# Kernel tuning notes

Measured on AMD Instinct MI355X. Metric: run time of the kernel, lower is better.

The kernel has to match this reference:

```python
import jax, jax.numpy as jnp
import numpy as np

NQ = 4          # n_qubits
NL = 2          # n_layers
DIM = 2 ** NQ   # statevector dimension (16)
PI = np.float32(np.pi)

# H^{otimes NQ} (real, symmetric)
_H2 = np.array([[1.0, 1.0], [1.0, -1.0]], dtype=np.float32) / np.sqrt(2.0)
_M = _H2
for _ in range(NQ - 1):
    _M = np.kron(_M, _H2)
H_ALL = jnp.asarray(_M.astype(np.complex64))  # [DIM, DIM]

# z_i = +1/-1 eigenvalues per computational basis state; wire 0 is MSB (PennyLane)
_b = ((np.arange(DIM)[:, None] >> (NQ - 1 - np.arange(NQ))[None, :]) & 1)
Z = jnp.asarray((1.0 - 2.0 * _b).astype(np.float32))      # [DIM, NQ]
ZZ = Z[:, :-1] * Z[:, 1:]                                  # [DIM, NQ-1]


def _encode(angles):
    """Apply the ZZ feature map to |0...0>. angles: [..., NQ] -> state [..., DIM] complex64.

    Per layer: all Hadamards, then diagonal phase exp(-i/2 (sum th_i z_i + sum th_i th_{i+1} z_i z_{i+1}))
    (RZ and CNOT-RZ-CNOT = ZZ phase are diagonal; gates on distinct wires commute).
    """
    arg = (jnp.einsum('...q,dq->...d', angles, Z)
           + jnp.einsum('...p,dp->...d', angles[..., :-1] * angles[..., 1:], ZZ))
    diag = jnp.exp(arg * (-0.5j)).astype(jnp.complex64)     # [..., DIM]
    state = jnp.zeros(angles.shape[:-1] + (DIM,), jnp.complex64).at[..., 0].set(1.0)
    for _ in range(NL):
        state = state @ H_ALL      # H_ALL symmetric -> s @ H == H @ s
        state = state * diag
    return state


def setup_inputs() -> dict:
    key = jax.random.key(0)
    ks = jax.random.split(key, 7)
    B, L, S, H, D = 8, 1024, 1024, 8, 64
    return {
        'queries': jax.random.normal(ks[0], (B, L, H, D), jnp.float32),
        'keys':    jax.random.normal(ks[1], (B, S, H, D), jnp.float32),
        'values':  jax.random.normal(ks[2], (B, S, H, D), jnp.float32),
        'wq': jax.random.normal(ks[3], (NQ, D), jnp.float32) * 0.1,
        'bq': jax.random.normal(ks[4], (NQ,), jnp.float32) * 0.1,
        'wk': jax.random.normal(ks[5], (NQ, D), jnp.float32) * 0.1,
        'bk': jax.random.normal(ks[6], (NQ,), jnp.float32) * 0.1,
    }


def reference(queries, keys, values, wq, bq, wk, bk):
    # queries: [B,L,H,D], keys/values: [B,S,H,D]
    q_angles = jnp.tanh(queries @ wq.T + bq) * PI          # [B,L,H,NQ]
    k_angles = jnp.tanh(keys @ wk.T + bk) * PI             # [B,S,H,NQ]
    sq = _encode(q_angles.transpose(0, 2, 1, 3))           # [B,H,L,DIM] complex
    sk = _encode(k_angles.transpose(0, 2, 1, 3))           # [B,H,S,DIM] complex
    fid = jnp.einsum('bhld,bhsd->bhls', sq, jnp.conj(sk))  # overlap <phi_k|phi_q>
    attn_scores = (fid.real ** 2 + fid.imag ** 2).astype(queries.dtype)  # |.|^2 = probs[0]
    attn_weights = attn_scores / (attn_scores.sum(axis=-1, keepdims=True) + 1e-6)
    v = values.transpose(0, 2, 1, 3)                       # [B,H,S,D]
    context = jnp.einsum('bhls,bhsd->bhld', attn_weights, v).transpose(0, 2, 1, 3)
    return context, attn_weights
```

## Files before the change

### kernel.cpp

```cpp
#include <hip/hip_runtime.h>
#include <math.h>

#define PI_F 3.14159265358979323846f

constexpr int Bq = 8, Lq = 1024, Sq = 1024, Hq = 8, Dq = 64;

typedef short short8 __attribute__((ext_vector_type(8)));
typedef _Float16 half8 __attribute__((ext_vector_type(8)));
typedef float f4v __attribute__((ext_vector_type(4)));
typedef unsigned short ushort_t;

static __device__ __forceinline__ f4v mfma16h(half8 a, half8 b, f4v c) {
  return __builtin_amdgcn_mfma_f32_16x16x32_f16(a, b, c, 0, 0, 0);
}
static __device__ __forceinline__ half8 primefh(half8 q) {
  union { half8 h; short8 s; } in, out;
  in.h = q;
#pragma unroll
  for (int i = 0; i < 4; ++i) {
    out.s[2 * i]     = in.s[2 * i + 1];
    out.s[2 * i + 1] = (short)(((ushort_t)in.s[2 * i]) ^ 0x8000u);
  }
  return out.h;
}
static __device__ __forceinline__ unsigned pkh(float a, float b) {
  union { _Float16 h[2]; unsigned u; } p;
  p.h[0] = (_Float16)a; p.h[1] = (_Float16)b;
  return p.u;
}

static __device__ __forceinline__ void state_vec(
    const float* __restrict__ x, const float (*lw)[64], const float* lb,
    int n, float st[32])
{
  const float4* xp = (const float4*)(x + (size_t)n * 64);
  float a0 = lb[0], a1 = lb[1], a2 = lb[2], a3 = lb[3];
#pragma unroll
  for (int i = 0; i < 16; ++i) {
    float4 v = xp[i];
    a0 += v.x * lw[0][4*i] + v.y * lw[0][4*i+1] + v.z * lw[0][4*i+2] + v.w * lw[0][4*i+3];
    a1 += v.x * lw[1][4*i] + v.y * lw[1][4*i+1] + v.z * lw[1][4*i+2] + v.w * lw[1][4*i+3];
    a2 += v.x * lw[2][4*i] + v.y * lw[2][4*i+1] + v.z * lw[2][4*i+2] + v.w * lw[2][4*i+3];
    a3 += v.x * lw[3][4*i] + v.y * lw[3][4*i+1] + v.z * lw[3][4*i+2] + v.w * lw[3][4*i+3];
  }
  a0 = tanhf(a0) * PI_F; a1 = tanhf(a1) * PI_F;
  a2 = tanhf(a2) * PI_F; a3 = tanhf(a3) * PI_F;
  float p01 = a0 * a1, p12 = a1 * a2, p23 = a2 * a3;

  float dr[16], di[16];
#pragma unroll
  for (int d = 0; d < 16; ++d) {
    float s0 = (d & 8) ? -1.f : 1.f;
    float s1 = (d & 4) ? -1.f : 1.f;
    float s2 = (d & 2) ? -1.f : 1.f;
    float s3 = (d & 1) ? -1.f : 1.f;
    float arg = a0*s0 + a1*s1 + a2*s2 + a3*s3
              + p01*s0*s1 + p12*s1*s2 + p23*s2*s3;
    float sn, cs;
    sincosf(0.5f * arg, &sn, &cs);
    dr[d] = cs; di[d] = -sn;
  }
  float hr[16], hi[16];
#pragma unroll
  for (int i = 0; i < 16; ++i) { hr[i] = dr[i]; hi[i] = di[i]; }
#pragma unroll
  for (int stp = 1; stp < 16; stp <<= 1) {
#pragma unroll
    for (int i = 0; i < 16; ++i) {
      if (!(i & stp)) {
        float xr = hr[i], yr = hr[i + stp];
        hr[i] = xr + yr; hr[i + stp] = xr - yr;
        float xi = hi[i], yi = hi[i + stp];
        hi[i] = xi + yi; hi[i + stp] = xi - yi;
      }
    }
  }
#pragma unroll
  for (int d = 0; d < 16; ++d) {
    st[2*d]   = (dr[d] * hr[d] - di[d] * hi[d]) * 0.0625f;
    st[2*d+1] = (dr[d] * hi[d] + di[d] * hr[d]) * 0.0625f;
  }
}

__global__ __launch_bounds__(256) void k_prep(
    const float* __restrict__ qin, const float* __restrict__ kin,
    const float* __restrict__ vin,
    const float* __restrict__ wq, const float* __restrict__ bq,
    const float* __restrict__ wk, const float* __restrict__ bk,
    ushort_t* __restrict__ QF, ushort_t* __restrict__ KF,
    ushort_t* __restrict__ VF)
{
  __shared__ float smem[64 * 68];
  int blk = blockIdx.x;
  int t = threadIdx.x;

  if (blk < 512) {
    const bool isQ = (blk < 256);
    const float* x    = isQ ? qin : kin;
    const float* w    = isQ ? wq : wk;
    const float* bias = isQ ? bq : bk;
    float (*lw)[64] = (float(*)[64])smem;
    float* lb = smem + 256;
    lw[t >> 6][t & 63] = w[t];
    if (t < 4) lb[t] = bias[t];
    __syncthreads();

    int n = (blk & 255) * 256 + t;
    float st[32];
    state_vec(x, lw, lb, n, st);
    int b = n >> 13, l = (n >> 3) & 1023, h = n & 7;
    int bh = b * 8 + h;

    unsigned hp[16];
#pragma unroll
    for (int i = 0; i < 16; ++i) hp[i] = pkh(st[2*i], st[2*i+1]);

    if (isQ) {
      size_t rb = ((size_t)bh * Lq + l) * 32;
      uint4* ph = (uint4*)(QF + rb);
#pragma unroll
      for (int i = 0; i < 4; ++i)
        ph[i] = make_uint4(hp[4*i], hp[4*i+1], hp[4*i+2], hp[4*i+3]);
    } else {
      int sf = l >> 4, lh = l & 15;
      size_t fb = (size_t)(bh * 64 + sf) * 512;
#pragma unroll
      for (int g = 0; g < 4; ++g) {
        size_t o = fb + (size_t)((g << 4) + lh) * 8;
        *(uint4*)(KF + o) = make_uint4(hp[4*g], hp[4*g+1], hp[4*g+2], hp[4*g+3]);
      }
    }
  } else {
    int blk2 = blk - 512;
    int bh = blk2 >> 4, c = blk2 & 15;
    int b = bh >> 3, h = bh & 7;
    int s0 = c << 6;
    int sl = t >> 2, dq = (t & 3) << 4;
    const float4* src =
        (const float4*)(vin + (((size_t)b * Sq + s0 + sl) * Hq + h) * 64 + dq);
#pragma unroll
    for (int i = 0; i < 4; ++i)
      *(float4*)&smem[sl * 68 + dq + 4 * i] = src[i];
    __syncthreads();
#pragma unroll
    for (int sidx = 0; sidx < 2; ++sidx) {
      int slot = sidx * 256 + t;
      int ks = slot >> 8, f2 = (slot >> 6) & 3, lane = slot & 63;
      int lh = lane & 15, g = lane >> 4;
      int d = f2 * 16 + lh;
      unsigned w4[4];
#pragma unroll
      for (int e2 = 0; e2 < 4; ++e2) {
        int sl0 = ks * 32 + g * 8 + 2 * e2;
        w4[e2] = pkh(smem[sl0 * 68 + d], smem[(sl0 + 1) * 68 + d]);
      }
      size_t off = ((((size_t)(bh * 16 + c) * 2 + ks) * 4 + f2) * 64 + lane) * 8;
      *(uint4*)(VF + off) = make_uint4(w4[0], w4[1], w4[2], w4[3]);
    }
  }
}

__global__ __launch_bounds__(256, 4) void k_fidpv7(
    const ushort_t* __restrict__ QF, const ushort_t* __restrict__ KF,
    const ushort_t* __restrict__ VF, float* __restrict__ attn,
    float* __restrict__ ctx)
{
  __shared__ float Wtr[4][16 * 68];

  int bid = blockIdx.x;
  int xcd = bid & 7, idx = bid >> 3;
  int bh = (xcd << 3) | (idx >> 4);
  int l0 = (idx & 15) << 6;
  int t = threadIdx.x;
  int wv = t >> 6, lane = t & 63;
  int lh = lane & 15, g = lane >> 4, ko = g << 3;
  int rowbase = l0 + (wv << 4);

  size_t qoff = ((size_t)bh * Lq + rowbase + lh) * 32 + ko;
  half8 qf  = *(const half8*)(QF + qoff);
  half8 qpf = primefh(qf);

  const ushort_t* gK = KF + (size_t)bh * 32768 + (size_t)lane * 8;
  const ushort_t* gV = VF + (size_t)bh * 65536 + (size_t)lane * 8;

  f4v zero = {0.f, 0.f, 0.f, 0.f};

  float rsum = 0.f;
#pragma unroll 8
  for (int sf = 0; sf < 64; ++sf) {
    half8 kf = *(const half8*)(gK + sf * 512);
    f4v fr = mfma16h(kf, qf, zero);
    f4v fi = mfma16h(kf, qpf, zero);
#pragma unroll
    for (int r = 0; r < 4; ++r) rsum += fr[r]*fr[r] + fi[r]*fi[r];
  }
  rsum += __shfl_xor(rsum, 16);
  rsum += __shfl_xor(rsum, 32);
  float rinv = 1.f / (rsum + 1e-6f);

  float* abase = attn + ((size_t)bh * Lq + rowbase) * Sq;
  float* wtr = &Wtr[wv][0];
  f4v acc[4] = {zero, zero, zero, zero};

  half8 kA[4], kB[4];
#pragma unroll
  for (int f = 0; f < 4; ++f)
    kA[f] = *(const half8*)(gK + f * 512);

#pragma unroll
  for (int c = 0; c < 16; ++c) {
    const bool even = !(c & 1);
    half8* kcur = even ? kA : kB;
    half8* knxt = even ? kB : kA;
    if (c < 15) {
#pragma unroll
      for (int f = 0; f < 4; ++f)
        knxt[f] = *(const half8*)(gK + ((c + 1) * 4 + f) * 512);
    }
    half8 vb[2][4];
#pragma unroll
    for (int ks = 0; ks < 2; ++ks)
#pragma unroll
      for (int f2 = 0; f2 < 4; ++f2)
        vb[ks][f2] = *(const half8*)(gV + (size_t)(((c*2+ks)*4+f2)) * 512);

#pragma unroll
    for (int f = 0; f < 4; ++f) {
      f4v fr = mfma16h(kcur[f], qf, zero);
      f4v fi = mfma16h(kcur[f], qpf, zero);
      f4v wv4;
#pragma unroll
      for (int r = 0; r < 4; ++r)
        wv4[r] = (fr[r]*fr[r] + fi[r]*fi[r]) * rinv;
      *(f4v*)&wtr[lh * 68 + (f << 4) + (g << 2)] = wv4;
    }
#pragma unroll
    for (int j = 0; j < 4; ++j) {
      int rowp = (j << 2) + g;
      f4v vv = *(const f4v*)&wtr[rowp * 68 + (lh << 2)];
      __builtin_nontemporal_store(
          vv, (f4v*)(abase + (size_t)rowp * Sq + (c << 6) + (lh << 2)));
    }
#pragma unroll
    for (int ks = 0; ks < 2; ++ks) {
      f4v w0 = *(const f4v*)&wtr[lh * 68 + (ks << 5) + ko];
      f4v w1 = *(const f4v*)&wtr[lh * 68 + (ks << 5) + ko + 4];
      half8 wh;
#pragma unroll
      for (int e = 0; e < 4; ++e) wh[e] = (_Float16)w0[e];
#pragma unroll
      for (int e = 0; e < 4; ++e) wh[4 + e] = (_Float16)w1[e];
#pragma unroll
      for (int f2 = 0; f2 < 4; ++f2)
        acc[f2] = mfma16h(wh, vb[ks][f2], acc[f2]);
    }
  }

  int b = bh >> 3, h = bh & 7;
#pragma unroll
  for (int f2 = 0; f2 < 4; ++f2) {
    int d = (f2 << 4) + lh;
#pragma unroll
    for (int r = 0; r < 4; ++r) {
      int l = rowbase + (g << 2) + r;
      ctx[(((size_t)b * Lq + l) * Hq + h) * 64 + d] = acc[f2][r];
    }
  }
}

extern "C" void kernel_launch(void* const* d_in, const int* in_sizes, int n_in,
                              void* d_out, int out_size, void* d_ws, size_t ws_size,
                              hipStream_t stream) {
  const float* q  = (const float*)d_in[0];
  const float* k  = (const float*)d_in[1];
  const float* v  = (const float*)d_in[2];
  const float* wq = (const float*)d_in[3];
  const float* bq = (const float*)d_in[4];
  const float* wk = (const float*)d_in[5];
  const float* bk = (const float*)d_in[6];

  float* out  = (float*)d_out;
  float* ctx  = out;
  float* attn = out + 4194304;

  char* wsb = (char*)d_ws;
  ushort_t* QF = (ushort_t*)(wsb);
  ushort_t* KF = (ushort_t*)(wsb + (size_t)4 * 1024 * 1024);
  ushort_t* VF = (ushort_t*)(wsb + (size_t)8 * 1024 * 1024);

  hipLaunchKernelGGL(k_prep, dim3(1536), dim3(256), 0, stream,
                     q, k, v, wq, bq, wk, bk, QF, KF, VF);
  hipLaunchKernelGGL(k_fidpv7, dim3(1024), dim3(256), 0, stream,
                     QF, KF, VF, attn, ctx);
}
```

Measured before the change: 87.30 us.

## Process two 16-row query tiles per wave to reuse K/V fragment loads

Each wave now handles 32 query rows (two 16-row tiles) instead of 16, so every K and V fragment loaded from global memory feeds twice as many MFMAs. The grid is halved to 512 blocks, each covering 128 rows, and launch bounds drop from 4 to 2 blocks per CU to make room for the doubled accumulators and the larger LDS staging buffer. The goal is to cut redundant K/V global traffic per output row. In exchange there is less occupancy and fewer blocks (512 across the CUs), which may hurt latency hiding, and the kernel is likely bound by the attention-weight write stream anyway.

```diff
diff --git a/kernel.cpp b/kernel.cpp
--- a/kernel.cpp
+++ b/kernel.cpp
@@ -160,47 +160,58 @@
   }
 }
 
-__global__ __launch_bounds__(256, 4) void k_fidpv7(
+__global__ __launch_bounds__(256, 2) void k_fidpv10(
     const ushort_t* __restrict__ QF, const ushort_t* __restrict__ KF,
     const ushort_t* __restrict__ VF, float* __restrict__ attn,
     float* __restrict__ ctx)
 {
-  __shared__ float Wtr[4][16 * 68];
+  __shared__ float Wtr[4][2][16 * 68];
 
   int bid = blockIdx.x;
   int xcd = bid & 7, idx = bid >> 3;
-  int bh = (xcd << 3) | (idx >> 4);
-  int l0 = (idx & 15) << 6;
+  int bh = (xcd << 3) | (idx >> 3);
+  int l0 = (idx & 7) << 7;
   int t = threadIdx.x;
   int wv = t >> 6, lane = t & 63;
   int lh = lane & 15, g = lane >> 4, ko = g << 3;
-  int rowbase = l0 + (wv << 4);
-
-  size_t qoff = ((size_t)bh * Lq + rowbase + lh) * 32 + ko;
-  half8 qf  = *(const half8*)(QF + qoff);
-  half8 qpf = primefh(qf);
+  int rowA = l0 + (wv << 5);
+  int rowB = rowA + 16;
+
+  size_t qoffA = ((size_t)bh * Lq + rowA + lh) * 32 + ko;
+  half8 qfA = *(const half8*)(QF + qoffA);
+  half8 qfB = *(const half8*)(QF + qoffA + 16 * 32);
+  half8 qpA = primefh(qfA), qpB = primefh(qfB);
 
   const ushort_t* gK = KF + (size_t)bh * 32768 + (size_t)lane * 8;
   const ushort_t* gV = VF + (size_t)bh * 65536 + (size_t)lane * 8;
 
   f4v zero = {0.f, 0.f, 0.f, 0.f};
 
-  float rsum = 0.f;
+  float rsA = 0.f, rsB = 0.f;
 #pragma unroll 8
   for (int sf = 0; sf < 64; ++sf) {
     half8 kf = *(const half8*)(gK + sf * 512);
-    f4v fr = mfma16h(kf, qf, zero);
-    f4v fi = mfma16h(kf, qpf, zero);
-#pragma unroll
-    for (int r = 0; r < 4; ++r) rsum += fr[r]*fr[r] + fi[r]*fi[r];
-  }
-  rsum += __shfl_xor(rsum, 16);
-  rsum += __shfl_xor(rsum, 32);
-  float rinv = 1.f / (rsum + 1e-6f);
-
-  float* abase = attn + ((size_t)bh * Lq + rowbase) * Sq;
-  float* wtr = &Wtr[wv][0];
-  f4v acc[4] = {zero, zero, zero, zero};
+    f4v frA = mfma16h(kf, qfA, zero);
+    f4v fiA = mfma16h(kf, qpA, zero);
+    f4v frB = mfma16h(kf, qfB, zero);
+    f4v fiB = mfma16h(kf, qpB, zero);
+#pragma unroll
+    for (int r = 0; r < 4; ++r) {
+      rsA += frA[r]*frA[r] + fiA[r]*fiA[r];
+      rsB += frB[r]*frB[r] + fiB[r]*fiB[r];
+    }
+  }
+  rsA += __shfl_xor(rsA, 16); rsA += __shfl_xor(rsA, 32);
+  rsB += __shfl_xor(rsB, 16); rsB += __shfl_xor(rsB, 32);
+  float rinvA = 1.f / (rsA + 1e-6f);
+  float rinvB = 1.f / (rsB + 1e-6f);
+
+  float* abA = attn + ((size_t)bh * Lq + rowA) * Sq;
+  float* abB = attn + ((size_t)bh * Lq + rowB) * Sq;
+  float* wtrA = &Wtr[wv][0][0];
+  float* wtrB = &Wtr[wv][1][0];
+  f4v accA[4] = {zero, zero, zero, zero};
+  f4v accB[4] = {zero, zero, zero, zero};
 
   half8 kA[4], kB[4];
 #pragma unroll
@@ -226,33 +237,46 @@
 
 #pragma unroll
     for (int f = 0; f < 4; ++f) {
-      f4v fr = mfma16h(kcur[f], qf, zero);
-      f4v fi = mfma16h(kcur[f], qpf, zero);
-      f4v wv4;
-#pragma unroll
-      for (int r = 0; r < 4; ++r)
-        wv4[r] = (fr[r]*fr[r] + fi[r]*fi[r]) * rinv;
-      *(f4v*)&wtr[lh * 68 + (f << 4) + (g << 2)] = wv4;
+      f4v frA = mfma16h(kcur[f], qfA, zero);
+      f4v fiA = mfma16h(kcur[f], qpA, zero);
+      f4v frB = mfma16h(kcur[f], qfB, zero);
+      f4v fiB = mfma16h(kcur[f], qpB, zero);
+      f4v wA, wB;
+#pragma unroll
+      for (int r = 0; r < 4; ++r) {
+        wA[r] = (frA[r]*frA[r] + fiA[r]*fiA[r]) * rinvA;
+        wB[r] = (frB[r]*frB[r] + fiB[r]*fiB[r]) * rinvB;
+      }
+      *(f4v*)&wtrA[lh * 68 + (f << 4) + (g << 2)] = wA;
+      *(f4v*)&wtrB[lh * 68 + (f << 4) + (g << 2)] = wB;
     }
 #pragma unroll
     for (int j = 0; j < 4; ++j) {
       int rowp = (j << 2) + g;
-      f4v vv = *(const f4v*)&wtr[rowp * 68 + (lh << 2)];
+      f4v vA = *(const f4v*)&wtrA[rowp * 68 + (lh << 2)];
+      f4v vB = *(const f4v*)&wtrB[rowp * 68 + (lh << 2)];
       __builtin_nontemporal_store(
-          vv, (f4v*)(abase + (size_t)rowp * Sq + (c << 6) + (lh << 2)));
+          vA, (f4v*)(abA + (size_t)rowp * Sq + (c << 6) + (lh << 2)));
+      __builtin_nontemporal_store(
+          vB, (f4v*)(abB + (size_t)rowp * Sq + (c << 6) + (lh << 2)));
     }
 #pragma unroll
     for (int ks = 0; ks < 2; ++ks) {
-      f4v w0 = *(const f4v*)&wtr[lh * 68 + (ks << 5) + ko];
-      f4v w1 = *(const f4v*)&wtr[lh * 68 + (ks << 5) + ko + 4];
-      half8 wh;
-#pragma unroll
-      for (int e = 0; e < 4; ++e) wh[e] = (_Float16)w0[e];
-#pragma unroll
-      for (int e = 0; e < 4; ++e) wh[4 + e] = (_Float16)w1[e];
-#pragma unroll
-      for (int f2 = 0; f2 < 4; ++f2)
-        acc[f2] = mfma16h(wh, vb[ks][f2], acc[f2]);
+      f4v a0 = *(const f4v*)&wtrA[lh * 68 + (ks << 5) + ko];
+      f4v a1 = *(const f4v*)&wtrA[lh * 68 + (ks << 5) + ko + 4];
+      f4v b0 = *(const f4v*)&wtrB[lh * 68 + (ks << 5) + ko];
+      f4v b1 = *(const f4v*)&wtrB[lh * 68 + (ks << 5) + ko + 4];
+      half8 whA, whB;
+#pragma unroll
+      for (int e = 0; e < 4; ++e) {
+        whA[e] = (_Float16)a0[e]; whA[4 + e] = (_Float16)a1[e];
+        whB[e] = (_Float16)b0[e]; whB[4 + e] = (_Float16)b1[e];
+      }
+#pragma unroll
+      for (int f2 = 0; f2 < 4; ++f2) {
+        accA[f2] = mfma16h(whA, vb[ks][f2], accA[f2]);
+        accB[f2] = mfma16h(whB, vb[ks][f2], accB[f2]);
+      }
     }
   }
 
@@ -262,8 +286,10 @@
     int d = (f2 << 4) + lh;
 #pragma unroll
     for (int r = 0; r < 4; ++r) {
-      int l = rowbase + (g << 2) + r;
-      ctx[(((size_t)b * Lq + l) * Hq + h) * 64 + d] = acc[f2][r];
+      int lA = rowA + (g << 2) + r;
+      int lB = rowB + (g << 2) + r;
+      ctx[(((size_t)b * Lq + lA) * Hq + h) * 64 + d] = accA[f2][r];
+      ctx[(((size_t)b * Lq + lB) * Hq + h) * 64 + d] = accB[f2][r];
     }
   }
 }
@@ -290,6 +316,6 @@
 
   hipLaunchKernelGGL(k_prep, dim3(1536), dim3(256), 0, stream,
                      q, k, v, wq, bq, wk, bk, QF, KF, VF);
-  hipLaunchKernelGGL(k_fidpv7, dim3(1024), dim3(256), 0, stream,
+  hipLaunchKernelGGL(k_fidpv10, dim3(512), dim3(256), 0, stream,
                      QF, KF, VF, attn, ctx);
 }
```

Result: slower. 99.46 us (+13.9%).

## Replace row-sum MFMA pass with precomputed key Gram matrix quadratic form

Applied to the files above, without the earlier changes.

Adds a k_csum kernel that builds, per (batch, head), a 32x32 Gram matrix of the encoded key states, folded so it also covers the imaginary part. The attention kernel now gets each row's normalizer as a quadratic form q^T C q instead of running a full extra MFMA sweep over all 1024 keys. This removes a second read of K and 128 MFMAs per wave before the main loop. The cost is an extra small kernel launch, 64 blocks of fp32 Gram work over K, and an fp32 workspace read. It also assumes the |fid|^2 sum factors exactly through this folding.

```diff
diff --git a/kernel.cpp b/kernel.cpp
--- a/kernel.cpp
+++ b/kernel.cpp
@@ -160,12 +160,64 @@
   }
 }
 
-__global__ __launch_bounds__(256, 4) void k_fidpv7(
+__global__ __launch_bounds__(256) void k_csum(
+    const ushort_t* __restrict__ KF, float* __restrict__ Cp)
+{
+  __shared__ float L[128][33];
+  __shared__ float Ct[32][33];
+  int bh = blockIdx.x;
+  int t = threadIdx.x;
+  const ushort_t* kb = KF + (size_t)bh * 32768;
+  int i = t >> 3, j0 = (t & 7) << 2;
+  float c0 = 0.f, c1 = 0.f, c2 = 0.f, c3 = 0.f;
+
+  for (int ch = 0; ch < 8; ++ch) {
+    __syncthreads();
+    {
+      const half8* src = (const half8*)(kb + ch * 4096 + t * 16);
+      half8 h0 = src[0], h1 = src[1];
+      int sf_l = t >> 5;
+      int pr = t & 31;
+      int lane0 = pr * 2, lane1 = lane0 + 1;
+      int s0 = sf_l * 16 + (lane0 & 15), d0 = (lane0 >> 4) * 8;
+      int s1 = sf_l * 16 + (lane1 & 15), d1 = (lane1 >> 4) * 8;
+#pragma unroll
+      for (int e = 0; e < 8; ++e) L[s0][d0 + e] = (float)h0[e];
+#pragma unroll
+      for (int e = 0; e < 8; ++e) L[s1][d1 + e] = (float)h1[e];
+    }
+    __syncthreads();
+#pragma unroll 4
+    for (int s = 0; s < 128; ++s) {
+      float a = L[s][i];
+      c0 += a * L[s][j0 + 0];
+      c1 += a * L[s][j0 + 1];
+      c2 += a * L[s][j0 + 2];
+      c3 += a * L[s][j0 + 3];
+    }
+  }
+  Ct[i][j0 + 0] = c0; Ct[i][j0 + 1] = c1;
+  Ct[i][j0 + 2] = c2; Ct[i][j0 + 3] = c3;
+  __syncthreads();
+  float ta = (i & 1) ? 1.f : -1.f;
+  float d4[4];
+#pragma unroll
+  for (int e = 0; e < 4; ++e) {
+    int b = j0 + e;
+    float tb = (b & 1) ? 1.f : -1.f;
+    d4[e] = Ct[i][b] + ta * tb * Ct[i ^ 1][b ^ 1];
+  }
+  *(float4*)(Cp + (size_t)bh * 1024 + i * 32 + j0) =
+      make_float4(d4[0], d4[1], d4[2], d4[3]);
+}
+
+__global__ __launch_bounds__(256, 4) void k_fidpv11(
     const ushort_t* __restrict__ QF, const ushort_t* __restrict__ KF,
-    const ushort_t* __restrict__ VF, float* __restrict__ attn,
-    float* __restrict__ ctx)
+    const ushort_t* __restrict__ VF, const float* __restrict__ Cp,
+    float* __restrict__ attn, float* __restrict__ ctx)
 {
   __shared__ float Wtr[4][16 * 68];
+  __shared__ float Dl[32 * 33];
 
   int bid = blockIdx.x;
   int xcd = bid & 7, idx = bid >> 3;
@@ -176,27 +228,42 @@
   int lh = lane & 15, g = lane >> 4, ko = g << 3;
   int rowbase = l0 + (wv << 4);
 
-  size_t qoff = ((size_t)bh * Lq + rowbase + lh) * 32 + ko;
-  half8 qf  = *(const half8*)(QF + qoff);
+#pragma unroll
+  for (int r = 0; r < 4; ++r) {
+    int idxq = r * 256 + t;
+    Dl[(idxq >> 5) * 33 + (idxq & 31)] = Cp[(size_t)bh * 1024 + idxq];
+  }
+  __syncthreads();
+
+  size_t qrowoff = ((size_t)bh * Lq + rowbase + lh) * 32;
+  const half8* qrow = (const half8*)(QF + qrowoff);
+  float q32[32];
+#pragma unroll
+  for (int w = 0; w < 4; ++w) {
+    half8 hv = qrow[w];
+#pragma unroll
+    for (int e = 0; e < 8; ++e) q32[w * 8 + e] = (float)hv[e];
+  }
+  float partial = 0.f;
+#pragma unroll
+  for (int il = 0; il < 8; ++il) {
+    int i = ko + il;
+    float y = 0.f;
+#pragma unroll
+    for (int j = 0; j < 32; ++j) y += Dl[i * 33 + j] * q32[j];
+    partial += q32[i] * y;
+  }
+  partial += __shfl_xor(partial, 16);
+  partial += __shfl_xor(partial, 32);
+  float rinv = 1.f / (partial + 1e-6f);
+
+  half8 qf  = qrow[g];
   half8 qpf = primefh(qf);
 
   const ushort_t* gK = KF + (size_t)bh * 32768 + (size_t)lane * 8;
   const ushort_t* gV = VF + (size_t)bh * 65536 + (size_t)lane * 8;
 
   f4v zero = {0.f, 0.f, 0.f, 0.f};
-
-  float rsum = 0.f;
-#pragma unroll 8
-  for (int sf = 0; sf < 64; ++sf) {
-    half8 kf = *(const half8*)(gK + sf * 512);
-    f4v fr = mfma16h(kf, qf, zero);
-    f4v fi = mfma16h(kf, qpf, zero);
-#pragma unroll
-    for (int r = 0; r < 4; ++r) rsum += fr[r]*fr[r] + fi[r]*fi[r];
-  }
-  rsum += __shfl_xor(rsum, 16);
-  rsum += __shfl_xor(rsum, 32);
-  float rinv = 1.f / (rsum + 1e-6f);
 
   float* abase = attn + ((size_t)bh * Lq + rowbase) * Sq;
   float* wtr = &Wtr[wv][0];
@@ -287,9 +354,11 @@
   ushort_t* QF = (ushort_t*)(wsb);
   ushort_t* KF = (ushort_t*)(wsb + (size_t)4 * 1024 * 1024);
   ushort_t* VF = (ushort_t*)(wsb + (size_t)8 * 1024 * 1024);
+  float*    Cp = (float*)(wsb + (size_t)16 * 1024 * 1024);
 
   hipLaunchKernelGGL(k_prep, dim3(1536), dim3(256), 0, stream,
                      q, k, v, wq, bq, wk, bk, QF, KF, VF);
-  hipLaunchKernelGGL(k_fidpv7, dim3(1024), dim3(256), 0, stream,
-                     QF, KF, VF, attn, ctx);
-}
+  hipLaunchKernelGGL(k_csum, dim3(64), dim3(256), 0, stream, KF, Cp);
+  hipLaunchKernelGGL(k_fidpv11, dim3(1024), dim3(256), 0, stream,
+                     QF, KF, VF, Cp, attn, ctx);
+}
```

Measured after the change: 113.6 us. +30.1%, slower.
